# Optimization experiments

Measured on AMD Instinct MI355X. Metric: run time of the kernel, lower is better.

Reference implementation:

```python
import jax, jax.numpy as jnp
import numpy as np

N = 50000      # nodes
E = 800000     # edges
DIM = 64       # node feature dim (= out_channels per head)
H = 4          # attention heads
EDGE_DIM = 3
LN_EPS = 1e-5
SLOPE = 0.2    # leaky relu negative slope (GATv2 default and FFN)


def _ln(x, g, b):
    mu = jnp.mean(x, axis=-1, keepdims=True)
    var = jnp.mean(jnp.square(x - mu), axis=-1, keepdims=True)
    return (x - mu) * jax.lax.rsqrt(var + LN_EPS) * g + b


def setup_inputs() -> dict:
    key = jax.random.key(0)
    ks = jax.random.split(key, 10)
    def g(k, shape, s=0.05):
        return jax.random.normal(k, shape, dtype=jnp.float32) * s
    return {
        "x": g(ks[0], (N, DIM), 1.0),
        "edge_index": jax.random.randint(ks[1], (2, E), 0, N),
        "edge_attr": g(ks[2], (E, EDGE_DIM), 1.0),
        # GATv2Conv params (lin_l, lin_r with bias; lin_edge no bias; att; out bias)
        "Wl": g(ks[3], (DIM, H * DIM)), "bl": jnp.zeros((H * DIM,), jnp.float32),
        "Wr": g(ks[4], (DIM, H * DIM)), "br": jnp.zeros((H * DIM,), jnp.float32),
        "We": g(ks[5], (EDGE_DIM, H * DIM)),
        "att_w": g(ks[6], (H, DIM)),
        "gat_b": jnp.zeros((DIM,), jnp.float32),
        # LayerNorms
        "ln1_g": jnp.ones((DIM,), jnp.float32), "ln1_b": jnp.zeros((DIM,), jnp.float32),
        "ln2_g": jnp.ones((DIM,), jnp.float32), "ln2_b": jnp.zeros((DIM,), jnp.float32),
        # FFN
        "W1": g(ks[7], (DIM, 2 * DIM)), "b1": jnp.zeros((2 * DIM,), jnp.float32),
        "W2": g(ks[8], (2 * DIM, DIM)), "b2": jnp.zeros((DIM,), jnp.float32),
    }


def _gatv2(x, edge_index, edge_attr, Wl, bl, Wr, br, We, att_w, gat_b):
    n = x.shape[0]
    src, dst = edge_index[0], edge_index[1]
    # add self loops; edge_attr fill_value='mean' (PyG default): per-target mean
    ea_sum = jax.ops.segment_sum(edge_attr, dst, num_segments=n)
    cnt = jax.ops.segment_sum(jnp.ones((edge_attr.shape[0], 1), edge_attr.dtype), dst, num_segments=n)
    loop_attr = ea_sum / jnp.maximum(cnt, 1.0)
    loop = jnp.arange(n)
    src = jnp.concatenate([src, loop])
    dst = jnp.concatenate([dst, loop])
    ea = jnp.concatenate([edge_attr, loop_attr], axis=0)
    # projections: [N,H,C]
    xl = (x @ Wl + bl).reshape(n, H, DIM)
    xr = (x @ Wr + br).reshape(n, H, DIM)
    ee = (ea @ We).reshape(-1, H, DIM)      # [E+N,H,C]
    z = jax.nn.leaky_relu(xl[src] + xr[dst] + ee, SLOPE)
    logits = jnp.einsum('ehc,hc->eh', z, att_w)   # [E+N,H]
    m = jax.ops.segment_max(logits, dst, num_segments=n)
    e = jnp.exp(logits - m[dst])
    denom = jax.ops.segment_sum(e, dst, num_segments=n)
    alpha = e / denom[dst]                         # segment softmax over targets
    out = jax.ops.segment_sum(alpha[:, :, None] * xl[src], dst, num_segments=n)
    return out.mean(axis=1) + gat_b               # concat=False -> head mean


def reference(x, edge_index, edge_attr, Wl, bl, Wr, br, We, att_w, gat_b,
              ln1_g, ln1_b, ln2_g, ln2_b, W1, b1, W2, b2):
    h = x + _gatv2(x, edge_index, edge_attr, Wl, bl, Wr, br, We, att_w, gat_b)
    h = _ln(h, ln1_g, ln1_b)
    ffn = jax.nn.leaky_relu(h @ W1 + b1, SLOPE) @ W2 + b2
    h = _ln(h + ffn, ln2_g, ln2_b)
    return h
```

## Files before the change

kernel.cpp:

```cpp
#include <hip/hip_runtime.h>
#include <hip/hip_fp16.h>

#ifndef __has_builtin
#define __has_builtin(x) 0
#endif

#define N_NODES 50000
#define N_EDGES 800000
#define DIM 64
#define NH 4
#define LN_EPS 1e-5f
#define SLOPE 0.2f
#define LOG2E 1.44269504f
#define PBLOCKS 512
#define PTILES 7
#define BCAP 64

__device__ __forceinline__ float lrelu(float v){ return v > 0.f ? v : SLOPE * v; }

__device__ __forceinline__ float waveSum64(float v){
  v += __shfl_xor(v, 1);  v += __shfl_xor(v, 2);  v += __shfl_xor(v, 4);
  v += __shfl_xor(v, 8);  v += __shfl_xor(v, 16); v += __shfl_xor(v, 32);
  return v;
}

__device__ __forceinline__ __half2 u2h2(unsigned u){ union{unsigned u; __half2 h;} c; c.u = u; return c.h; }
__device__ __forceinline__ unsigned h22u(__half2 h){ union{unsigned u; __half2 h;} c; c.h = h; return c.u; }

__device__ __forceinline__ __half2 hmax2(__half2 a, __half2 b){
  unsigned ua = h22u(a), ub = h22u(b), r;
  asm("v_pk_max_f16 %0, %1, %2" : "=v"(r) : "v"(ua), "v"(ub));
  return u2h2(r);
}

__device__ __forceinline__ float fdot2f(unsigned a, unsigned b, float c){
#if __has_builtin(__builtin_amdgcn_fdot2)
  typedef _Float16 h2v __attribute__((ext_vector_type(2)));
  union U{unsigned u; h2v h;};
  U ua, ub; ua.u = a; ub.u = b;
  return __builtin_amdgcn_fdot2(ua.h, ub.h, c, false);
#else
  float r;
  asm("v_dot2_f32_f16 %0, %1, %2, %3" : "=v"(r) : "v"(a), "v"(b), "v"(c));
  return r;
#endif
}

__device__ __forceinline__ float exp2fast(float x){
#if __has_builtin(__builtin_amdgcn_exp2f)
  return __builtin_amdgcn_exp2f(x);
#else
  float r; asm("v_exp_f32 %0, %1" : "=v"(r) : "v"(x)); return r;
#endif
}

__device__ __forceinline__ float sum16fast(float v){
  asm("s_nop 1\n\t"
      "v_add_f32_dpp %0, %0, %0 quad_perm:[1,0,3,2] row_mask:0xf bank_mask:0xf\n\t"
      "s_nop 1\n\t"
      "v_add_f32_dpp %0, %0, %0 quad_perm:[2,3,0,1] row_mask:0xf bank_mask:0xf\n\t"
      "s_nop 1\n\t"
      "v_add_f32_dpp %0, %0, %0 row_ror:4 row_mask:0xf bank_mask:0xf\n\t"
      "s_nop 1\n\t"
      "v_add_f32_dpp %0, %0, %0 row_ror:8 row_mask:0xf bank_mask:0xf"
      : "+v"(v));
  return v;
}

__device__ __forceinline__ void sum16quad(float& a, float& b, float& c, float& d){
  asm("v_add_f32_dpp %0, %0, %0 quad_perm:[1,0,3,2] row_mask:0xf bank_mask:0xf\n\t"
      "v_add_f32_dpp %1, %1, %1 quad_perm:[1,0,3,2] row_mask:0xf bank_mask:0xf\n\t"
      "v_add_f32_dpp %2, %2, %2 quad_perm:[1,0,3,2] row_mask:0xf bank_mask:0xf\n\t"
      "v_add_f32_dpp %3, %3, %3 quad_perm:[1,0,3,2] row_mask:0xf bank_mask:0xf\n\t"
      "v_add_f32_dpp %0, %0, %0 quad_perm:[2,3,0,1] row_mask:0xf bank_mask:0xf\n\t"
      "v_add_f32_dpp %1, %1, %1 quad_perm:[2,3,0,1] row_mask:0xf bank_mask:0xf\n\t"
      "v_add_f32_dpp %2, %2, %2 quad_perm:[2,3,0,1] row_mask:0xf bank_mask:0xf\n\t"
      "v_add_f32_dpp %3, %3, %3 quad_perm:[2,3,0,1] row_mask:0xf bank_mask:0xf\n\t"
      "v_add_f32_dpp %0, %0, %0 row_ror:4 row_mask:0xf bank_mask:0xf\n\t"
      "v_add_f32_dpp %1, %1, %1 row_ror:4 row_mask:0xf bank_mask:0xf\n\t"
      "v_add_f32_dpp %2, %2, %2 row_ror:4 row_mask:0xf bank_mask:0xf\n\t"
      "v_add_f32_dpp %3, %3, %3 row_ror:4 row_mask:0xf bank_mask:0xf\n\t"
      "v_add_f32_dpp %0, %0, %0 row_ror:8 row_mask:0xf bank_mask:0xf\n\t"
      "v_add_f32_dpp %1, %1, %1 row_ror:8 row_mask:0xf bank_mask:0xf\n\t"
      "v_add_f32_dpp %2, %2, %2 row_ror:8 row_mask:0xf bank_mask:0xf\n\t"
      "v_add_f32_dpp %3, %3, %3 row_ror:8 row_mask:0xf bank_mask:0xf"
      : "+v"(a), "+v"(b), "+v"(c), "+v"(d));
}

__global__ __launch_bounds__(256)
void proj_kernel(const float* __restrict__ x,
                 const float* __restrict__ Wl, const float* __restrict__ bl,
                 const float* __restrict__ Wr, const float* __restrict__ br,
                 __half* __restrict__ xlh, __half* __restrict__ xrh,
                 const int* __restrict__ ei, const float* __restrict__ ea,
                 int* __restrict__ cursor, uint2* __restrict__ buckets,
                 const float* __restrict__ W1, const float* __restrict__ W2,
                 unsigned* __restrict__ W1p, unsigned* __restrict__ W2p){
  __shared__ uint2 wlds[32][256];
  __shared__ unsigned xs2[16][32];
  const int tid = threadIdx.x;
  const int cp = tid & 127;
  const bool isL = tid < 128;
  const float* Wb = isL ? Wl : Wr;
  const float* bb = isL ? bl : br;
  for (int kk = 0; kk < 32; ++kk){
    float2 a0 = *(const float2*)&Wb[(2 * kk) * 256 + 2 * cp];
    float2 a1 = *(const float2*)&Wb[(2 * kk + 1) * 256 + 2 * cp];
    uint2 w;
    w.x = h22u(__floats2half2_rn(a0.x, a1.x));
    w.y = h22u(__floats2half2_rn(a0.y, a1.y));
    wlds[kk][tid] = w;
  }
  const float bA = bb[2 * cp], bB = bb[2 * cp + 1];
  __half* outp = (isL ? xlh : xrh) + 2 * cp;
  for (int t = 0; t < PTILES; ++t){
    const int base = (blockIdx.x * PTILES + t) * 16;
    if (base >= N_NODES) break;
    __syncthreads();
    {
      int r = tid >> 4, q = tid & 15;
      int n = base + r;
      float4 v;
      if (n < N_NODES) v = *(const float4*)&x[(size_t)n * 64 + q * 4];
      else { v.x = 0.f; v.y = 0.f; v.z = 0.f; v.w = 0.f; }
      xs2[r][q * 2]     = h22u(__floats2half2_rn(v.x, v.y));
      xs2[r][q * 2 + 1] = h22u(__floats2half2_rn(v.z, v.w));
    }
    __syncthreads();
    float accA[16], accB[16];
#pragma unroll
    for (int i = 0; i < 16; ++i){ accA[i] = bA; accB[i] = bB; }
    for (int k4 = 0; k4 < 8; ++k4){
      const uint2 w0 = wlds[k4 * 4 + 0][tid];
      const uint2 w1 = wlds[k4 * 4 + 1][tid];
      const uint2 w2 = wlds[k4 * 4 + 2][tid];
      const uint2 w3 = wlds[k4 * 4 + 3][tid];
#pragma unroll
      for (int i = 0; i < 16; ++i){
        uint4 xv = *(const uint4*)&xs2[i][k4 * 4];
        accA[i] = fdot2f(xv.x, w0.x, accA[i]);
        accB[i] = fdot2f(xv.x, w0.y, accB[i]);
        accA[i] = fdot2f(xv.y, w1.x, accA[i]);
        accB[i] = fdot2f(xv.y, w1.y, accB[i]);
        accA[i] = fdot2f(xv.z, w2.x, accA[i]);
        accB[i] = fdot2f(xv.z, w2.y, accB[i]);
        accA[i] = fdot2f(xv.w, w3.x, accA[i]);
        accB[i] = fdot2f(xv.w, w3.y, accB[i]);
      }
    }
#pragma unroll
    for (int i = 0; i < 16; ++i){
      if (base + i < N_NODES)
        *(unsigned*)(outp + (size_t)(base + i) * 256) =
            h22u(__floats2half2_rn(accA[i], accB[i]));
    }
  }
  const int gid0 = blockIdx.x * 256 + tid;
  if (gid0 < 4096){
    int kk = gid0 >> 7, cc = gid0 & 127;
    W1p[gid0] = h22u(__floats2half2_rn(W1[(2 * kk) * 128 + cc], W1[(2 * kk + 1) * 128 + cc]));
  } else if (gid0 < 8192){
    int j = gid0 - 4096;
    int kk = j >> 6, cc = j & 63;
    W2p[j] = h22u(__floats2half2_rn(W2[(2 * kk) * 64 + cc], W2[(2 * kk + 1) * 64 + cc]));
  }
  for (int e = gid0; e < N_EDGES; e += PBLOCKS * 256){
    int dst = ei[N_EDGES + e];
    int pos = atomicAdd(&cursor[dst], 1);
    pos = min(pos, BCAP - 1);
    uint2 v;
    v.x = h22u(__floats2half2_rn(ea[e * 3 + 0], ea[e * 3 + 1]));
    v.y = (h22u(__floats2half2_rn(ea[e * 3 + 2], 0.f)) & 0xffffu) | ((unsigned)ei[e] << 16);
    buckets[(size_t)dst * BCAP + pos] = v;
  }
}

#define EDGE_MATH(he0, he1, he2, a01, a23, p)                                        \
  {                                                                                  \
    __half2 z01 = __hadd2(a01, xr01);                                                \
    z01 = __hfma2(u2h2(he0), w0a, z01);                                              \
    z01 = __hfma2(u2h2(he1), w1a, z01);                                              \
    z01 = __hfma2(u2h2(he2), w2a, z01);                                              \
    __half2 z23 = __hadd2(a23, xr23);                                                \
    z23 = __hfma2(u2h2(he0), w0b, z23);                                              \
    z23 = __hfma2(u2h2(he1), w1b, z23);                                              \
    z23 = __hfma2(u2h2(he2), w2b, z23);                                              \
    z01 = hmax2(z01, __hmul2(z01, slp));                                             \
    z23 = hmax2(z23, __hmul2(z23, slp));                                             \
    p = fdot2f(h22u(z01), awa, fdot2f(h22u(z23), awb, 0.f));                         \
  }

__global__ __launch_bounds__(64)
void aggregate_kernel(const int* __restrict__ cursor, const uint2* __restrict__ buckets,
                      const __half* __restrict__ xlh, const __half* __restrict__ xrh,
                      const float* __restrict__ We, const float* __restrict__ att,
                      const float* __restrict__ x, const float* __restrict__ gat_b,
                      const float* __restrict__ ln1g, const float* __restrict__ ln1b,
                      __half* __restrict__ h1h){
  const int n = blockIdx.x;
  const int lane = threadIdx.x;
  const int j0 = lane * 4;
  const unsigned awa = h22u(__floats2half2_rn(att[j0] * LOG2E, att[j0 + 1] * LOG2E));
  const unsigned awb = h22u(__floats2half2_rn(att[j0 + 2] * LOG2E, att[j0 + 3] * LOG2E));
  const __half2 w0a = __floats2half2_rn(We[j0], We[j0 + 1]);
  const __half2 w0b = __floats2half2_rn(We[j0 + 2], We[j0 + 3]);
  const __half2 w1a = __floats2half2_rn(We[256 + j0], We[256 + j0 + 1]);
  const __half2 w1b = __floats2half2_rn(We[256 + j0 + 2], We[256 + j0 + 3]);
  const __half2 w2a = __floats2half2_rn(We[512 + j0], We[512 + j0 + 1]);
  const __half2 w2b = __floats2half2_rn(We[512 + j0 + 2], We[512 + j0 + 3]);
  const __half2 slp = __float2half2_rn(SLOPE);
  uint2 uxr = *(const uint2*)(xrh + (size_t)n * 256 + j0);
  const __half2 xr01 = u2h2(uxr.x), xr23 = u2h2(uxr.y);

  __half2 acc01 = __float2half2_rn(0.f), acc23 = __float2half2_rn(0.f);
  float den = 0.f;
  const int deg = min(cursor[n], BCAP);
  uint2 m2; m2.x = 0; m2.y = 0;
  if (lane < deg) m2 = buckets[(size_t)n * BCAP + lane];
  float s0 = __low2float(u2h2(m2.x));
  float s1 = __high2float(u2h2(m2.x));
  float s2 = __low2float(u2h2(m2.y & 0xffffu));
  int j = 0;
  for (; j + 4 <= deg; j += 4){
    const unsigned sxA = (unsigned)__builtin_amdgcn_readlane((int)m2.x, j);
    const unsigned syA = (unsigned)__builtin_amdgcn_readlane((int)m2.y, j);
    const unsigned sxB = (unsigned)__builtin_amdgcn_readlane((int)m2.x, j + 1);
    const unsigned syB = (unsigned)__builtin_amdgcn_readlane((int)m2.y, j + 1);
    const unsigned sxC = (unsigned)__builtin_amdgcn_readlane((int)m2.x, j + 2);
    const unsigned syC = (unsigned)__builtin_amdgcn_readlane((int)m2.y, j + 2);
    const unsigned sxD = (unsigned)__builtin_amdgcn_readlane((int)m2.x, j + 3);
    const unsigned syD = (unsigned)__builtin_amdgcn_readlane((int)m2.y, j + 3);
    uint2 uA = *(const uint2*)(xlh + (size_t)(syA >> 16) * 256 + j0);
    uint2 uB = *(const uint2*)(xlh + (size_t)(syB >> 16) * 256 + j0);
    uint2 uC = *(const uint2*)(xlh + (size_t)(syC >> 16) * 256 + j0);
    uint2 uD = *(const uint2*)(xlh + (size_t)(syD >> 16) * 256 + j0);
    const unsigned heA0 = (sxA & 0xffffu) | (sxA << 16), heA1 = (sxA >> 16) | (sxA & 0xffff0000u), heA2 = (syA & 0xffffu) | (syA << 16);
    const unsigned heB0 = (sxB & 0xffffu) | (sxB << 16), heB1 = (sxB >> 16) | (sxB & 0xffff0000u), heB2 = (syB & 0xffffu) | (syB << 16);
    const unsigned heC0 = (sxC & 0xffffu) | (sxC << 16), heC1 = (sxC >> 16) | (sxC & 0xffff0000u), heC2 = (syC & 0xffffu) | (syC << 16);
    const unsigned heD0 = (sxD & 0xffffu) | (sxD << 16), heD1 = (sxD >> 16) | (sxD & 0xffff0000u), heD2 = (syD & 0xffffu) | (syD << 16);
    const __half2 aA01 = u2h2(uA.x), aA23 = u2h2(uA.y);
    const __half2 aB01 = u2h2(uB.x), aB23 = u2h2(uB.y);
    const __half2 aC01 = u2h2(uC.x), aC23 = u2h2(uC.y);
    const __half2 aD01 = u2h2(uD.x), aD23 = u2h2(uD.y);
    float pA, pB, pC, pD;
    EDGE_MATH(heA0, heA1, heA2, aA01, aA23, pA)
    EDGE_MATH(heB0, heB1, heB2, aB01, aB23, pB)
    EDGE_MATH(heC0, heC1, heC2, aC01, aC23, pC)
    EDGE_MATH(heD0, heD1, heD2, aD01, aD23, pD)
    sum16quad(pA, pB, pC, pD);
    float wA = exp2fast(pA), wB = exp2fast(pB);
    float wC = exp2fast(pC), wD = exp2fast(pD);
    __half2 whA = __float2half2_rn(wA), whB = __float2half2_rn(wB);
    __half2 whC = __float2half2_rn(wC), whD = __float2half2_rn(wD);
    acc01 = __hfma2(whA, aA01, acc01); acc23 = __hfma2(whA, aA23, acc23);
    acc01 = __hfma2(whB, aB01, acc01); acc23 = __hfma2(whB, aB23, acc23);
    acc01 = __hfma2(whC, aC01, acc01); acc23 = __hfma2(whC, aC23, acc23);
    acc01 = __hfma2(whD, aD01, acc01); acc23 = __hfma2(whD, aD23, acc23);
    den += (wA + wB) + (wC + wD);
  }
  for (; j < deg; ++j){
    const unsigned sx = (unsigned)__builtin_amdgcn_readlane((int)m2.x, j);
    const unsigned sy = (unsigned)__builtin_amdgcn_readlane((int)m2.y, j);
    const unsigned he0 = (sx & 0xffffu) | (sx << 16);
    const unsigned he1 = (sx >> 16) | (sx & 0xffff0000u);
    const unsigned he2 = (sy & 0xffffu) | (sy << 16);
    uint2 u = *(const uint2*)(xlh + (size_t)(sy >> 16) * 256 + j0);
    const __half2 a01 = u2h2(u.x), a23 = u2h2(u.y);
    float p;
    EDGE_MATH(he0, he1, he2, a01, a23, p)
    p = sum16fast(p);
    float w = exp2fast(p);
    __half2 wh = __float2half2_rn(w);
    acc01 = __hfma2(wh, a01, acc01);
    acc23 = __hfma2(wh, a23, acc23);
    den += w;
  }

  {
    const float inv = 1.f / (float)max(deg, 1);
    const float e0 = waveSum64(s0) * inv;
    const float e1 = waveSum64(s1) * inv;
    const float e2 = waveSum64(s2) * inv;
    const __half2 he0h = __float2half2_rn(e0), he1h = __float2half2_rn(e1), he2h = __float2half2_rn(e2);
    uint2 u = *(const uint2*)(xlh + (size_t)n * 256 + j0);
    const __half2 a01 = u2h2(u.x), a23 = u2h2(u.y);
    __half2 z01 = __hadd2(a01, xr01);
    z01 = __hfma2(he0h, w0a, z01); z01 = __hfma2(he1h, w1a, z01); z01 = __hfma2(he2h, w2a, z01);
    __half2 z23 = __hadd2(a23, xr23);
    z23 = __hfma2(he0h, w0b, z23); z23 = __hfma2(he1h, w1b, z23); z23 = __hfma2(he2h, w2b, z23);
    z01 = hmax2(z01, __hmul2(z01, slp));
    z23 = hmax2(z23, __hmul2(z23, slp));
    float p = fdot2f(h22u(z01), awa, fdot2f(h22u(z23), awb, 0.f));
    p = sum16fast(p);
    float w = exp2fast(p);
    __half2 wh = __float2half2_rn(w);
    acc01 = __hfma2(wh, a01, acc01);
    acc23 = __hfma2(wh, a23, acc23);
    den += w;
  }

  float rd = 1.f / den;
  float4 o;
  o.x = __low2float(acc01) * rd; o.y = __high2float(acc01) * rd;
  o.z = __low2float(acc23) * rd; o.w = __high2float(acc23) * rd;
  o.x += __shfl_xor(o.x, 16); o.x += __shfl_xor(o.x, 32);
  o.y += __shfl_xor(o.y, 16); o.y += __shfl_xor(o.y, 32);
  o.z += __shfl_xor(o.z, 16); o.z += __shfl_xor(o.z, 32);
  o.w += __shfl_xor(o.w, 16); o.w += __shfl_xor(o.w, 32);
  const int c0 = (lane & 15) * 4;
  const float4 xv = *(const float4*)(x + (size_t)n * 64 + c0);
  const float4 gb = *(const float4*)(gat_b + c0);
  o.x = 0.25f * o.x + gb.x + xv.x;
  o.y = 0.25f * o.y + gb.y + xv.y;
  o.z = 0.25f * o.z + gb.z + xv.z;
  o.w = 0.25f * o.w + gb.w + xv.w;
  float t1 = sum16fast(o.x + o.y + o.z + o.w);
  float mu = t1 * (1.f / 64.f);
  float4 d; d.x = o.x - mu; d.y = o.y - mu; d.z = o.z - mu; d.w = o.w - mu;
  float t2 = sum16fast(d.x * d.x + d.y * d.y + d.z * d.z + d.w * d.w);
  float rs = rsqrtf(t2 * (1.f / 64.f) + LN_EPS);
  if (lane < 16){
    const float4 g4 = *(const float4*)(ln1g + c0);
    const float4 b4 = *(const float4*)(ln1b + c0);
    uint2 r;
    r.x = h22u(__floats2half2_rn(d.x * rs * g4.x + b4.x, d.y * rs * g4.y + b4.y));
    r.y = h22u(__floats2half2_rn(d.z * rs * g4.z + b4.z, d.w * rs * g4.w + b4.w));
    *(uint2*)(h1h + (size_t)n * 64 + c0) = r;
  }
}

#define FT 32
__global__ void ffn_kernel(const __half* __restrict__ h1h,
                           const unsigned* __restrict__ W1p, const float* __restrict__ b1,
                           const unsigned* __restrict__ W2p, const float* __restrict__ b2,
                           const float* __restrict__ ln2g, const float* __restrict__ ln2b,
                           float* __restrict__ out){
  __shared__ __half2 hs2[FT][32];
  __shared__ __half  ts1[FT][128];
  __shared__ float   fs[FT][64];
  const int base = blockIdx.x * FT;
  const int tid = threadIdx.x;
  for (int i = tid; i < FT * 32; i += 256){
    int r = i >> 5, cc = i & 31;
    int n = base + r;
    unsigned hu = 0;
    if (n < N_NODES) hu = ((const unsigned*)(h1h + (size_t)n * 64))[cc];
    __half2 hv = u2h2(hu);
    hs2[r][cc] = hv;
    fs[r][cc * 2] = __low2float(hv); fs[r][cc * 2 + 1] = __high2float(hv);
  }
  __syncthreads();
  {
    const int c1 = tid & 127, half = tid >> 7;
    __half2 acc[16];
#pragma unroll
    for (int i = 0; i < 16; ++i) acc[i] = __float2half2_rn(0.f);
    for (int kk = 0; kk < 32; kk += 2){
      __half2 wA = u2h2(W1p[(kk + 0) * 128 + c1]);
      __half2 wB = u2h2(W1p[(kk + 1) * 128 + c1]);
#pragma unroll
      for (int i = 0; i < 16; ++i){
        uint2 hv = *(const uint2*)&hs2[half * 16 + i][kk];
        acc[i] = __hfma2(u2h2(hv.x), wA, acc[i]);
        acc[i] = __hfma2(u2h2(hv.y), wB, acc[i]);
      }
    }
    const float b1c = b1[c1];
#pragma unroll
    for (int i = 0; i < 16; ++i){
      float t = __low2float(acc[i]) + __high2float(acc[i]) + b1c;
      ts1[half * 16 + i][c1] = __float2half(lrelu(t));
    }
  }
  __syncthreads();
  {
    const int c2 = tid & 63, qq = tid >> 6;
    __half2 acc2[8];
#pragma unroll
    for (int i = 0; i < 8; ++i) acc2[i] = __float2half2_rn(0.f);
    for (int kk = 0; kk < 64; kk += 2){
      __half2 wA = u2h2(W2p[(kk + 0) * 64 + c2]);
      __half2 wB = u2h2(W2p[(kk + 1) * 64 + c2]);
#pragma unroll
      for (int i = 0; i < 8; ++i){
        uint2 tt = *(const uint2*)&ts1[qq * 8 + i][2 * kk];
        acc2[i] = __hfma2(u2h2(tt.x), wA, acc2[i]);
        acc2[i] = __hfma2(u2h2(tt.y), wB, acc2[i]);
      }
    }
    const float b2c = b2[c2];
#pragma unroll
    for (int i = 0; i < 8; ++i)
      fs[qq * 8 + i][c2] += __low2float(acc2[i]) + __high2float(acc2[i]) + b2c;
  }
  __syncthreads();
  {
    const int lane = tid & 63, qq = tid >> 6;
    const float g = ln2g[lane], bb = ln2b[lane];
    for (int i = 0; i < 8; ++i){
      int r = qq * 8 + i;
      int n = base + r;
      if (n >= N_NODES) break;
      float v = fs[r][lane];
      float mu = waveSum64(v) * (1.f / 64.f);
      float dlt = v - mu;
      float var = waveSum64(dlt * dlt) * (1.f / 64.f);
      out[(size_t)n * 64 + lane] = dlt * rsqrtf(var + LN_EPS) * g + bb;
    }
  }
}

extern "C" void kernel_launch(void* const* d_in, const int* in_sizes, int n_in,
                              void* d_out, int out_size, void* d_ws, size_t ws_size,
                              hipStream_t stream){
  const float* x     = (const float*)d_in[0];
  const int*   ei    = (const int*)  d_in[1];
  const float* ea    = (const float*)d_in[2];
  const float* Wl    = (const float*)d_in[3];
  const float* bl    = (const float*)d_in[4];
  const float* Wr    = (const float*)d_in[5];
  const float* br    = (const float*)d_in[6];
  const float* We    = (const float*)d_in[7];
  const float* att   = (const float*)d_in[8];
  const float* gat_b = (const float*)d_in[9];
  const float* ln1g  = (const float*)d_in[10];
  const float* ln1b  = (const float*)d_in[11];
  const float* ln2g  = (const float*)d_in[12];
  const float* ln2b  = (const float*)d_in[13];
  const float* W1    = (const float*)d_in[14];
  const float* b1    = (const float*)d_in[15];
  const float* W2    = (const float*)d_in[16];
  const float* b2    = (const float*)d_in[17];
  float* out = (float*)d_out;

  uint2*    buckets = (uint2*)d_ws;
  __half*   xlh     = (__half*)(buckets + (size_t)N_NODES * BCAP);
  __half*   xrh     = xlh + (size_t)N_NODES * 256;
  __half*   h1h     = xrh + (size_t)N_NODES * 256;
  int*      cursor  = (int*)(h1h + (size_t)N_NODES * 64);
  unsigned* W1p     = (unsigned*)(cursor + N_NODES);
  unsigned* W2p     = W1p + 4096;

  (void)hipMemsetAsync(cursor, 0, (size_t)N_NODES * sizeof(int), stream);

  proj_kernel<<<PBLOCKS, 256, 0, stream>>>(x, Wl, bl, Wr, br, xlh, xrh,
                                           ei, ea, cursor, buckets, W1, W2, W1p, W2p);
  aggregate_kernel<<<N_NODES, 64, 0, stream>>>(
      cursor, buckets, xlh, xrh, We, att, x, gat_b, ln1g, ln1b, h1h);
  ffn_kernel<<<(N_NODES + FT - 1) / FT, 256, 0, stream>>>(h1h, W1p, b1, W2p, b2, ln2g, ln2b, out);
}
```

Before: 177.3 us.

## Interleave edge bucketing with projection tiles and widen per-thread output columns

Restructures the projection kernel so each thread computes 4 output columns across 16 nodes, with 32-node tiles and weights packed as uint4 over 8 k-values. The edge bucket scatter is moved into the tile loop: edge loads and cursor atomics are issued before the dot-product math and the bucket stores after it, to hide their latency behind compute. This raises register pressure (64 accumulators) and changes the LDS layout, in exchange for better weight reuse and overlap of memory-bound scatter with ALU work.

```diff
diff --git a/kernel.cpp b/kernel.cpp
--- a/kernel.cpp
+++ b/kernel.cpp
@@ -13,7 +13,7 @@
 #define SLOPE 0.2f
 #define LOG2E 1.44269504f
 #define PBLOCKS 512
-#define PTILES 7
+#define PTILES 4
 #define BCAP 64
 
 __device__ __forceinline__ float lrelu(float v){ return v > 0.f ? v : SLOPE * v; }
@@ -96,63 +96,24 @@
                  int* __restrict__ cursor, uint2* __restrict__ buckets,
                  const float* __restrict__ W1, const float* __restrict__ W2,
                  unsigned* __restrict__ W1p, unsigned* __restrict__ W2p){
-  __shared__ uint2 wlds[32][256];
-  __shared__ unsigned xs2[16][32];
+  __shared__ uint4 wq[8][128][4];
+  __shared__ unsigned xs2[32][32];
   const int tid = threadIdx.x;
-  const int cp = tid & 127;
-  const bool isL = tid < 128;
-  const float* Wb = isL ? Wl : Wr;
-  const float* bb = isL ? bl : br;
-  for (int kk = 0; kk < 32; ++kk){
-    float2 a0 = *(const float2*)&Wb[(2 * kk) * 256 + 2 * cp];
-    float2 a1 = *(const float2*)&Wb[(2 * kk + 1) * 256 + 2 * cp];
-    uint2 w;
-    w.x = h22u(__floats2half2_rn(a0.x, a1.x));
-    w.y = h22u(__floats2half2_rn(a0.y, a1.y));
-    wlds[kk][tid] = w;
-  }
-  const float bA = bb[2 * cp], bB = bb[2 * cp + 1];
-  __half* outp = (isL ? xlh : xrh) + 2 * cp;
-  for (int t = 0; t < PTILES; ++t){
-    const int base = (blockIdx.x * PTILES + t) * 16;
-    if (base >= N_NODES) break;
-    __syncthreads();
-    {
-      int r = tid >> 4, q = tid & 15;
-      int n = base + r;
-      float4 v;
-      if (n < N_NODES) v = *(const float4*)&x[(size_t)n * 64 + q * 4];
-      else { v.x = 0.f; v.y = 0.f; v.z = 0.f; v.w = 0.f; }
-      xs2[r][q * 2]     = h22u(__floats2half2_rn(v.x, v.y));
-      xs2[r][q * 2 + 1] = h22u(__floats2half2_rn(v.z, v.w));
-    }
-    __syncthreads();
-    float accA[16], accB[16];
-#pragma unroll
-    for (int i = 0; i < 16; ++i){ accA[i] = bA; accB[i] = bB; }
-    for (int k4 = 0; k4 < 8; ++k4){
-      const uint2 w0 = wlds[k4 * 4 + 0][tid];
-      const uint2 w1 = wlds[k4 * 4 + 1][tid];
-      const uint2 w2 = wlds[k4 * 4 + 2][tid];
-      const uint2 w3 = wlds[k4 * 4 + 3][tid];
-#pragma unroll
-      for (int i = 0; i < 16; ++i){
-        uint4 xv = *(const uint4*)&xs2[i][k4 * 4];
-        accA[i] = fdot2f(xv.x, w0.x, accA[i]);
-        accB[i] = fdot2f(xv.x, w0.y, accB[i]);
-        accA[i] = fdot2f(xv.y, w1.x, accA[i]);
-        accB[i] = fdot2f(xv.y, w1.y, accB[i]);
-        accA[i] = fdot2f(xv.z, w2.x, accA[i]);
-        accB[i] = fdot2f(xv.z, w2.y, accB[i]);
-        accA[i] = fdot2f(xv.w, w3.x, accA[i]);
-        accB[i] = fdot2f(xv.w, w3.y, accB[i]);
-      }
-    }
-#pragma unroll
-    for (int i = 0; i < 16; ++i){
-      if (base + i < N_NODES)
-        *(unsigned*)(outp + (size_t)(base + i) * 256) =
-            h22u(__floats2half2_rn(accA[i], accB[i]));
+  const int cq = tid & 127;
+  {
+    const int k4base = (tid >> 7) * 4;
+    for (int k4 = k4base; k4 < k4base + 4; ++k4){
+      for (int j = 0; j < 4; ++j){
+        const int g = 4 * cq + j;
+        const float* Wb = (g < 256) ? Wl : Wr;
+        const int col = g & 255;
+        uint4 v;
+        v.x = h22u(__floats2half2_rn(Wb[(k4 * 8 + 0) * 256 + col], Wb[(k4 * 8 + 1) * 256 + col]));
+        v.y = h22u(__floats2half2_rn(Wb[(k4 * 8 + 2) * 256 + col], Wb[(k4 * 8 + 3) * 256 + col]));
+        v.z = h22u(__floats2half2_rn(Wb[(k4 * 8 + 4) * 256 + col], Wb[(k4 * 8 + 5) * 256 + col]));
+        v.w = h22u(__floats2half2_rn(Wb[(k4 * 8 + 6) * 256 + col], Wb[(k4 * 8 + 7) * 256 + col]));
+        wq[k4][cq][j] = v;
+      }
     }
   }
   const int gid0 = blockIdx.x * 256 + tid;
@@ -164,14 +125,101 @@
     int kk = j >> 6, cc = j & 63;
     W2p[j] = h22u(__floats2half2_rn(W2[(2 * kk) * 64 + cc], W2[(2 * kk + 1) * 64 + cc]));
   }
-  for (int e = gid0; e < N_EDGES; e += PBLOCKS * 256){
-    int dst = ei[N_EDGES + e];
-    int pos = atomicAdd(&cursor[dst], 1);
-    pos = min(pos, BCAP - 1);
-    uint2 v;
-    v.x = h22u(__floats2half2_rn(ea[e * 3 + 0], ea[e * 3 + 1]));
-    v.y = (h22u(__floats2half2_rn(ea[e * 3 + 2], 0.f)) & 0xffffu) | ((unsigned)ei[e] << 16);
-    buckets[(size_t)dst * BCAP + pos] = v;
+  float bias[4];
+#pragma unroll
+  for (int j = 0; j < 4; ++j){
+    const int g = 4 * cq + j;
+    bias[j] = (g < 256) ? bl[g] : br[g - 256];
+  }
+  const int g0 = 4 * cq;
+  __half* outp = (g0 < 256) ? (xlh + g0) : (xrh + g0 - 256);
+  const int nodeoff = (tid >> 7) * 16;
+
+  for (int t = 0; t < PTILES; ++t){
+    const int base = (blockIdx.x * PTILES + t) * 32;
+    __syncthreads();
+    if (base < N_NODES){
+#pragma unroll
+      for (int s = 0; s < 2; ++s){
+        int flat = s * 256 + tid;
+        int r = flat >> 4, q = flat & 15;
+        int n = base + r;
+        float4 v;
+        if (n < N_NODES) v = *(const float4*)&x[(size_t)n * 64 + q * 4];
+        else { v.x = 0.f; v.y = 0.f; v.z = 0.f; v.w = 0.f; }
+        xs2[r][q * 2]     = h22u(__floats2half2_rn(v.x, v.y));
+        xs2[r][q * 2 + 1] = h22u(__floats2half2_rn(v.z, v.w));
+      }
+    }
+    __syncthreads();
+    const int e0i = (t * PBLOCKS + blockIdx.x) * 512 + tid;
+    const int e1i = e0i + 256;
+    const bool h0 = e0i < N_EDGES, h1 = e1i < N_EDGES;
+    const int ec0 = h0 ? e0i : 0, ec1 = h1 ? e1i : 0;
+    const int dst0 = ei[N_EDGES + ec0], src0 = ei[ec0];
+    const int dst1 = ei[N_EDGES + ec1], src1 = ei[ec1];
+    const float a00 = ea[ec0 * 3 + 0], a01 = ea[ec0 * 3 + 1], a02 = ea[ec0 * 3 + 2];
+    const float a10 = ea[ec1 * 3 + 0], a11 = ea[ec1 * 3 + 1], a12 = ea[ec1 * 3 + 2];
+    int pos0 = 0, pos1 = 0;
+    if (h0) pos0 = atomicAdd(&cursor[dst0], 1);
+    if (h1) pos1 = atomicAdd(&cursor[dst1], 1);
+    if (base < N_NODES){
+      float acc0[16], acc1[16], acc2[16], acc3[16];
+#pragma unroll
+      for (int i = 0; i < 16; ++i){
+        acc0[i] = bias[0]; acc1[i] = bias[1]; acc2[i] = bias[2]; acc3[i] = bias[3];
+      }
+      for (int k4 = 0; k4 < 8; ++k4){
+        const uint4 w0 = wq[k4][cq][0];
+        const uint4 w1 = wq[k4][cq][1];
+        const uint4 w2 = wq[k4][cq][2];
+        const uint4 w3 = wq[k4][cq][3];
+#pragma unroll
+        for (int i = 0; i < 16; ++i){
+          const uint4 xv = *(const uint4*)&xs2[nodeoff + i][k4 * 4];
+          acc0[i] = fdot2f(xv.x, w0.x, acc0[i]);
+          acc0[i] = fdot2f(xv.y, w0.y, acc0[i]);
+          acc0[i] = fdot2f(xv.z, w0.z, acc0[i]);
+          acc0[i] = fdot2f(xv.w, w0.w, acc0[i]);
+          acc1[i] = fdot2f(xv.x, w1.x, acc1[i]);
+          acc1[i] = fdot2f(xv.y, w1.y, acc1[i]);
+          acc1[i] = fdot2f(xv.z, w1.z, acc1[i]);
+          acc1[i] = fdot2f(xv.w, w1.w, acc1[i]);
+          acc2[i] = fdot2f(xv.x, w2.x, acc2[i]);
+          acc2[i] = fdot2f(xv.y, w2.y, acc2[i]);
+          acc2[i] = fdot2f(xv.z, w2.z, acc2[i]);
+          acc2[i] = fdot2f(xv.w, w2.w, acc2[i]);
+          acc3[i] = fdot2f(xv.x, w3.x, acc3[i]);
+          acc3[i] = fdot2f(xv.y, w3.y, acc3[i]);
+          acc3[i] = fdot2f(xv.z, w3.z, acc3[i]);
+          acc3[i] = fdot2f(xv.w, w3.w, acc3[i]);
+        }
+      }
+#pragma unroll
+      for (int i = 0; i < 16; ++i){
+        const int n = base + nodeoff + i;
+        if (n < N_NODES){
+          uint2 r;
+          r.x = h22u(__floats2half2_rn(acc0[i], acc1[i]));
+          r.y = h22u(__floats2half2_rn(acc2[i], acc3[i]));
+          *(uint2*)(outp + (size_t)n * 256) = r;
+        }
+      }
+    }
+    if (h0){
+      int p = min(pos0, BCAP - 1);
+      uint2 v;
+      v.x = h22u(__floats2half2_rn(a00, a01));
+      v.y = (h22u(__floats2half2_rn(a02, 0.f)) & 0xffffu) | ((unsigned)src0 << 16);
+      buckets[(size_t)dst0 * BCAP + p] = v;
+    }
+    if (h1){
+      int p = min(pos1, BCAP - 1);
+      uint2 v;
+      v.x = h22u(__floats2half2_rn(a10, a11));
+      v.y = (h22u(__floats2half2_rn(a12, 0.f)) & 0xffffu) | ((unsigned)src1 << 16);
+      buckets[(size_t)dst1 * BCAP + p] = v;
+    }
   }
 }
 
```

After: 184.9 us. 1.04x slower.

## Use MFMA for node projections and overlap edge bucketing atomics with GEMM

Applied to the files above, without the earlier changes.

Replaces the LDS-staged fdot2 projection GEMM with MFMA 16x16x16 f16 instructions: each wave holds its B fragments in registers and reads x rows straight from global memory. Edge loads and cursor atomics are issued before the GEMM and the bucket stores after it, so atomic latency can hide behind the matrix work. The grid changes to 782 blocks of 64 nodes each, with four edges per thread. Output stores are scattered 2-byte half writes, which may coalesce less well than the previous packed half2 stores.

```diff
diff --git a/kernel.cpp b/kernel.cpp
--- a/kernel.cpp
+++ b/kernel.cpp
@@ -12,9 +12,11 @@
 #define LN_EPS 1e-5f
 #define SLOPE 0.2f
 #define LOG2E 1.44269504f
-#define PBLOCKS 512
-#define PTILES 7
+#define PBLOCKS 782
 #define BCAP 64
+
+typedef _Float16 half4v __attribute__((ext_vector_type(4)));
+typedef float floatx4 __attribute__((ext_vector_type(4)));
 
 __device__ __forceinline__ float lrelu(float v){ return v > 0.f ? v : SLOPE * v; }
 
@@ -96,65 +98,10 @@
                  int* __restrict__ cursor, uint2* __restrict__ buckets,
                  const float* __restrict__ W1, const float* __restrict__ W2,
                  unsigned* __restrict__ W1p, unsigned* __restrict__ W2p){
-  __shared__ uint2 wlds[32][256];
-  __shared__ unsigned xs2[16][32];
   const int tid = threadIdx.x;
-  const int cp = tid & 127;
-  const bool isL = tid < 128;
-  const float* Wb = isL ? Wl : Wr;
-  const float* bb = isL ? bl : br;
-  for (int kk = 0; kk < 32; ++kk){
-    float2 a0 = *(const float2*)&Wb[(2 * kk) * 256 + 2 * cp];
-    float2 a1 = *(const float2*)&Wb[(2 * kk + 1) * 256 + 2 * cp];
-    uint2 w;
-    w.x = h22u(__floats2half2_rn(a0.x, a1.x));
-    w.y = h22u(__floats2half2_rn(a0.y, a1.y));
-    wlds[kk][tid] = w;
-  }
-  const float bA = bb[2 * cp], bB = bb[2 * cp + 1];
-  __half* outp = (isL ? xlh : xrh) + 2 * cp;
-  for (int t = 0; t < PTILES; ++t){
-    const int base = (blockIdx.x * PTILES + t) * 16;
-    if (base >= N_NODES) break;
-    __syncthreads();
-    {
-      int r = tid >> 4, q = tid & 15;
-      int n = base + r;
-      float4 v;
-      if (n < N_NODES) v = *(const float4*)&x[(size_t)n * 64 + q * 4];
-      else { v.x = 0.f; v.y = 0.f; v.z = 0.f; v.w = 0.f; }
-      xs2[r][q * 2]     = h22u(__floats2half2_rn(v.x, v.y));
-      xs2[r][q * 2 + 1] = h22u(__floats2half2_rn(v.z, v.w));
-    }
-    __syncthreads();
-    float accA[16], accB[16];
-#pragma unroll
-    for (int i = 0; i < 16; ++i){ accA[i] = bA; accB[i] = bB; }
-    for (int k4 = 0; k4 < 8; ++k4){
-      const uint2 w0 = wlds[k4 * 4 + 0][tid];
-      const uint2 w1 = wlds[k4 * 4 + 1][tid];
-      const uint2 w2 = wlds[k4 * 4 + 2][tid];
-      const uint2 w3 = wlds[k4 * 4 + 3][tid];
-#pragma unroll
-      for (int i = 0; i < 16; ++i){
-        uint4 xv = *(const uint4*)&xs2[i][k4 * 4];
-        accA[i] = fdot2f(xv.x, w0.x, accA[i]);
-        accB[i] = fdot2f(xv.x, w0.y, accB[i]);
-        accA[i] = fdot2f(xv.y, w1.x, accA[i]);
-        accB[i] = fdot2f(xv.y, w1.y, accB[i]);
-        accA[i] = fdot2f(xv.z, w2.x, accA[i]);
-        accB[i] = fdot2f(xv.z, w2.y, accB[i]);
-        accA[i] = fdot2f(xv.w, w3.x, accA[i]);
-        accB[i] = fdot2f(xv.w, w3.y, accB[i]);
-      }
-    }
-#pragma unroll
-    for (int i = 0; i < 16; ++i){
-      if (base + i < N_NODES)
-        *(unsigned*)(outp + (size_t)(base + i) * 256) =
-            h22u(__floats2half2_rn(accA[i], accB[i]));
-    }
-  }
+  const int lane = tid & 63, w = tid >> 6;
+  const int row = lane & 15, kg = lane >> 4;
+
   const int gid0 = blockIdx.x * 256 + tid;
   if (gid0 < 4096){
     int kk = gid0 >> 7, cc = gid0 & 127;
@@ -164,14 +111,80 @@
     int kk = j >> 6, cc = j & 63;
     W2p[j] = h22u(__floats2half2_rn(W2[(2 * kk) * 64 + cc], W2[(2 * kk + 1) * 64 + cc]));
   }
-  for (int e = gid0; e < N_EDGES; e += PBLOCKS * 256){
-    int dst = ei[N_EDGES + e];
-    int pos = atomicAdd(&cursor[dst], 1);
-    pos = min(pos, BCAP - 1);
-    uint2 v;
-    v.x = h22u(__floats2half2_rn(ea[e * 3 + 0], ea[e * 3 + 1]));
-    v.y = (h22u(__floats2half2_rn(ea[e * 3 + 2], 0.f)) & 0xffffu) | ((unsigned)ei[e] << 16);
-    buckets[(size_t)dst * BCAP + pos] = v;
+
+  int edst[4], epos[4]; uint2 epk[4]; bool ehas[4];
+#pragma unroll
+  for (int q = 0; q < 4; ++q){
+    const int e = gid0 + q * (PBLOCKS * 256);
+    ehas[q] = e < N_EDGES;
+    const int ec = ehas[q] ? e : 0;
+    edst[q] = ei[N_EDGES + ec];
+    const int src = ei[ec];
+    const float e0 = ea[ec * 3 + 0], e1 = ea[ec * 3 + 1], e2 = ea[ec * 3 + 2];
+    epk[q].x = h22u(__floats2half2_rn(e0, e1));
+    epk[q].y = (h22u(__floats2half2_rn(e2, 0.f)) & 0xffffu) | ((unsigned)src << 16);
+    epos[q] = ehas[q] ? atomicAdd(&cursor[edst[q]], 1) : 0;
+  }
+
+  const int colb = w * 128;
+  const bool isL = colb < 256;
+  const float* Wb = isL ? Wl : Wr;
+  const float* bb = isL ? bl : br;
+  const int cl = colb & 255;
+  half4v bf[8][4];
+  float bias[8];
+#pragma unroll
+  for (int nt = 0; nt < 8; ++nt){
+    const int c = cl + nt * 16 + row;
+    bias[nt] = bb[c];
+#pragma unroll
+    for (int kc = 0; kc < 4; ++kc){
+      half4v b;
+#pragma unroll
+      for (int e = 0; e < 4; ++e)
+        b[e] = (_Float16)Wb[(kc * 16 + kg * 4 + e) * 256 + c];
+      bf[nt][kc] = b;
+    }
+  }
+  __half* outb = isL ? xlh : xrh;
+
+  const int nbase = blockIdx.x * 64;
+  for (int m = 0; m < 4; ++m){
+    const int nb = nbase + m * 16;
+    if (nb >= N_NODES) break;
+    const int nld = min(nb + row, N_NODES - 1);
+    half4v af[4];
+#pragma unroll
+    for (int kc = 0; kc < 4; ++kc){
+      const float4 xv = *(const float4*)&x[(size_t)nld * 64 + kc * 16 + kg * 4];
+      half4v a;
+      a[0] = (_Float16)xv.x; a[1] = (_Float16)xv.y;
+      a[2] = (_Float16)xv.z; a[3] = (_Float16)xv.w;
+      af[kc] = a;
+    }
+#pragma unroll
+    for (int nt = 0; nt < 8; ++nt){
+      floatx4 acc = {0.f, 0.f, 0.f, 0.f};
+      acc = __builtin_amdgcn_mfma_f32_16x16x16f16(af[0], bf[nt][0], acc, 0, 0, 0);
+      acc = __builtin_amdgcn_mfma_f32_16x16x16f16(af[1], bf[nt][1], acc, 0, 0, 0);
+      acc = __builtin_amdgcn_mfma_f32_16x16x16f16(af[2], bf[nt][2], acc, 0, 0, 0);
+      acc = __builtin_amdgcn_mfma_f32_16x16x16f16(af[3], bf[nt][3], acc, 0, 0, 0);
+      const int c = cl + nt * 16 + row;
+#pragma unroll
+      for (int r = 0; r < 4; ++r){
+        const int nrow = nb + kg * 4 + r;
+        if (nrow < N_NODES)
+          outb[(size_t)nrow * 256 + c] = __float2half(acc[r] + bias[nt]);
+      }
+    }
+  }
+
+#pragma unroll
+  for (int q = 0; q < 4; ++q){
+    if (ehas[q]){
+      const int p = min(epos[q], BCAP - 1);
+      buckets[(size_t)edst[q] * BCAP + p] = epk[q];
+    }
   }
 }
 
```

After: 165.4 us. -6.7%, faster.
